# Performance work log

Hardware: AMD Instinct MI355X
Metric: run time of the kernel (lower is better)

## Reference

```python
import jax, jax.numpy as jnp
import numpy as np

N = 1_000_000          # number of fusion candidate pairs
H, W = 200, 70400      # sparse buffer dims hard-coded in the module
FILL = -9999999.0


def _init_conv(k, co, ci):
    # torch Conv2d default init: U(-1/sqrt(fan_in), 1/sqrt(fan_in)), 1x1 kernel
    bound = 1.0 / np.sqrt(ci)
    kw, kb = jax.random.split(k)
    w = jax.random.uniform(kw, (co, ci), jnp.float32, -bound, bound)
    b = jax.random.uniform(kb, (co,), jnp.float32, -bound, bound)
    return w, b


def setup_inputs() -> dict:
    key = jax.random.key(0)
    ks = jax.random.split(key, 7)
    input_1 = jax.random.normal(ks[0], (1, 4, 1, N), dtype=jnp.float32)
    idx0 = jax.random.randint(ks[1], (N,), 0, H)   # row in [0,200)
    idx1 = jax.random.randint(ks[2], (N,), 0, W)   # col in [0,70400)
    tensor_index = jnp.stack([idx0, idx1], axis=1).astype(jnp.int64)
    w1, b1 = _init_conv(ks[3], 18, 4)
    w2, b2 = _init_conv(ks[4], 36, 18)
    w3, b3 = _init_conv(ks[5], 36, 36)
    w4, b4 = _init_conv(ks[6], 1, 36)
    return dict(input_1=input_1, tensor_index=tensor_index,
                w1=w1, b1=b1, w2=w2, b2=b2, w3=w3, b3=b3, w4=w4, b4=b4)


def _fuse_2d_3d(x, w1, b1, w2, b2, w3, b3, w4, b4):
    # x: (4, N); 1x1 convs over a (1,C,1,N) tensor == per-point channel matmuls
    h = jax.nn.relu(w1 @ x + b1[:, None])
    h = jax.nn.relu(w2 @ h + b2[:, None])
    h = jax.nn.relu(w3 @ h + b3[:, None])
    return w4 @ h + b4[:, None]  # (1, N)


def reference(input_1, tensor_index, w1, b1, w2, b2, w3, b3, w4, b4):
    base = jnp.full((1, H, W), FILL, dtype=input_1.dtype)

    def scatter_branch(_):
        feat = _fuse_2d_3d(input_1[0, :, 0, :], w1, b1, w2, b2, w3, b3, w4, b4)  # (1, N)
        out = base.at[:, tensor_index[:, 0], tensor_index[:, 1]].set(feat)
        return out, jnp.int32(1)

    def empty_branch(_):
        return base, jnp.int32(0)

    out_1, flag = jax.lax.cond(tensor_index[0, 0] == -1,
                               empty_branch, scatter_branch, None)
    # MaxPool2d([200,1]) over (C=1,H=200,W) -> max over H; squeeze+reshape -> (1, W, 1)
    x = jnp.max(out_1, axis=1)            # (1, W)
    return x.reshape(1, -1, 1), flag
```

## Files before the change

### kernel.cpp

```cpp
#include <hip/hip_runtime.h>

#define N_PTS 1000000
#define H_DIM 200
#define W_DIM 70400
#define FILL_V -9999999.0f

#define COUNTS_BYTES ((size_t)W_DIM * sizeof(int))
#define WPACK_ELEMS  6656
#define WPACK_BYTES  ((size_t)WPACK_ELEMS * 2)

typedef __attribute__((ext_vector_type(4))) float f32x4;
typedef __attribute__((ext_vector_type(8))) short bf16x8;

__device__ __forceinline__ unsigned bperm_u(unsigned src_lane, unsigned v) {
    return (unsigned)__builtin_amdgcn_ds_bpermute((int)(src_lane << 2), (int)v);
}
__device__ __forceinline__ unsigned cvt_pk_bf16(float lo, float hi) {
    unsigned d;
    asm("v_cvt_pk_bf16_f32 %0, %1, %2" : "=v"(d) : "v"(lo), "v"(hi));
    return d;
}
__device__ __forceinline__ bf16x8 mk_frag(unsigned d0, unsigned d1,
                                          unsigned d2, unsigned d3) {
    union { unsigned u[4]; bf16x8 s; } u;
    u.u[0] = d0; u.u[1] = d1; u.u[2] = d2; u.u[3] = d3;
    return u.s;
}

__global__ void __launch_bounds__(256) pack_weights_kernel(
    const float* __restrict__ w1, const float* __restrict__ b1,
    const float* __restrict__ w2, const float* __restrict__ b2,
    const float* __restrict__ w3, const float* __restrict__ b3,
    const float* __restrict__ w4, const float* __restrict__ b4,
    unsigned short* __restrict__ wp)
{
    for (int idx = threadIdx.x; idx < WPACK_ELEMS; idx += 256) {
        const int rem  = idx & 511;
        const int lane = rem >> 3, j = rem & 7;
        const int c16 = lane & 15, gk = lane >> 4;
        const int kloc = gk * 8 + j;
        float v = 0.0f;
        if (idx < 1024) {
            const int row = (idx >> 9) * 16 + c16, k = kloc;
            if (row < 18) v = (k < 4) ? w1[row * 4 + k] : (k == 4 ? b1[row] : 0.0f);
        } else if (idx < 2560) {
            const int row = ((idx - 1024) >> 9) * 16 + c16;
            const int f = (j < 4) ? (4 * gk + j) : (16 + 4 * gk + (j - 4));
            if (row < 36) v = (f < 18) ? w2[row * 18 + f] : (f == 18 ? b2[row] : 0.0f);
        } else if (idx < 5632) {
            const int f = (idx - 2560) >> 9;
            const int row = (f >> 1) * 16 + c16, k = (f & 1) * 32 + kloc;
            if (row < 36) v = (k < 36) ? w3[row * 36 + k] : (k == 36 ? b3[row] : 0.0f);
        } else {
            const int row = c16, k = ((idx - 5632) >> 9) * 32 + kloc;
            if (row == 0) v = (k < 36) ? w4[k] : (k == 36 ? b4[0] : 0.0f);
        }
        const unsigned b = __float_as_uint(v);
        wp[idx] = (unsigned short)((b + 0x7FFFu + ((b >> 16) & 1u)) >> 16);
    }
}

__global__ void __launch_bounds__(256) mlp_scatter_kernel(
    const float* __restrict__ input,
    const int* __restrict__ tindex,
    const unsigned short* __restrict__ wp,
    int* __restrict__ counts,
    uint2* __restrict__ list,
    int maxk)
{
    if (tindex[0] == -1) return;

    const int l   = threadIdx.x & 63;
    const int wav = (blockIdx.x * 256 + threadIdx.x) >> 6;
    const int base = wav << 6;
    if (base >= N_PTS) return;
    const int i = base + l;
    const int c16 = l & 15, g = l >> 4;

    const int2 hw = ((const int2*)tindex)[i];
    const int pos = atomicAdd(&counts[hw.y], 1);

    const bf16x8* __restrict__ wf = (const bf16x8*)wp;
    const bf16x8 A1_0 = wf[0 * 64 + l], A1_1 = wf[1 * 64 + l];
    const bf16x8 A2_0 = wf[2 * 64 + l], A2_1 = wf[3 * 64 + l], A2_2 = wf[4 * 64 + l];
    const bf16x8 A3_00 = wf[5 * 64 + l], A3_01 = wf[6 * 64 + l];
    const bf16x8 A3_10 = wf[7 * 64 + l], A3_11 = wf[8 * 64 + l];
    const bf16x8 A3_20 = wf[9 * 64 + l], A3_21 = wf[10 * 64 + l];
    const bf16x8 A4_0 = wf[11 * 64 + l], A4_1 = wf[12 * 64 + l];

    const f32x4 zf = {0.0f, 0.0f, 0.0f, 0.0f};

    const float x0 = input[0 * N_PTS + i], x1 = input[1 * N_PTS + i];
    const float x2 = input[2 * N_PTS + i], x3 = input[3 * N_PTS + i];
    const unsigned xp01 = cvt_pk_bf16(x0, x1);
    const unsigned xp23 = cvt_pk_bf16(x2, x3);

    unsigned P1[4][2][2];
#pragma unroll
    for (int t = 0; t < 4; ++t) {
        const unsigned srcl = (unsigned)(16 * t + c16);
        const unsigned bx0 = bperm_u(srcl, xp01);
        const unsigned bx1 = bperm_u(srcl, xp23);
        const unsigned d0 = (g == 0) ? bx0 : 0u;
        const unsigned d1 = (g == 0) ? bx1 : 0u;
        const unsigned d2 = (g == 0) ? 0x3F80u : 0u;
        const bf16x8 B = mk_frag(d0, d1, d2, 0u);
        const f32x4 D0 = __builtin_amdgcn_mfma_f32_16x16x32_bf16(A1_0, B, zf, 0, 0, 0);
        const f32x4 D1 = __builtin_amdgcn_mfma_f32_16x16x32_bf16(A1_1, B, zf, 0, 0, 0);
        P1[t][0][0] = cvt_pk_bf16(fmaxf(D0.x, 0.f), fmaxf(D0.y, 0.f));
        P1[t][0][1] = cvt_pk_bf16(fmaxf(D0.z, 0.f), fmaxf(D0.w, 0.f));
        P1[t][1][0] = cvt_pk_bf16(fmaxf(D1.x, 0.f), fmaxf(D1.y, 0.f));
        P1[t][1][1] = cvt_pk_bf16(fmaxf(D1.z, 0.f), fmaxf(D1.w, 0.f));
    }

    unsigned P2[4][3][2];
#pragma unroll
    for (int t = 0; t < 4; ++t) {
        const unsigned d0 = P1[t][0][0];
        const unsigned d1 = P1[t][0][1];
        const unsigned d2 = P1[t][1][0];
        const unsigned d3 = (g == 0) ? 0x3F80u
                                     : P1[t][1][1];
        const bf16x8 B = mk_frag(d0, d1, d2, d3);
        const f32x4 D0 = __builtin_amdgcn_mfma_f32_16x16x32_bf16(A2_0, B, zf, 0, 0, 0);
        const f32x4 D1 = __builtin_amdgcn_mfma_f32_16x16x32_bf16(A2_1, B, zf, 0, 0, 0);
        const f32x4 D2 = __builtin_amdgcn_mfma_f32_16x16x32_bf16(A2_2, B, zf, 0, 0, 0);
        P2[t][0][0] = cvt_pk_bf16(fmaxf(D0.x, 0.f), fmaxf(D0.y, 0.f));
        P2[t][0][1] = cvt_pk_bf16(fmaxf(D0.z, 0.f), fmaxf(D0.w, 0.f));
        P2[t][1][0] = cvt_pk_bf16(fmaxf(D1.x, 0.f), fmaxf(D1.y, 0.f));
        P2[t][1][1] = cvt_pk_bf16(fmaxf(D1.z, 0.f), fmaxf(D1.w, 0.f));
        P2[t][2][0] = cvt_pk_bf16(fmaxf(D2.x, 0.f), fmaxf(D2.y, 0.f));
        P2[t][2][1] = cvt_pk_bf16(fmaxf(D2.z, 0.f), fmaxf(D2.w, 0.f));
    }

    unsigned P3[4][3][2];
#pragma unroll
    for (int t = 0; t < 4; ++t) {
        unsigned dk0[4], dk1[4];
#pragma unroll
        for (int p = 0; p < 4; ++p) {
            const int Rl = (4 * g + p) & 7;
            const unsigned srcl = (unsigned)(c16 + 16 * (Rl >> 1));
            const unsigned lo = bperm_u(srcl, P2[t][0][p & 1]);
            const unsigned hi = bperm_u(srcl, P2[t][1][p & 1]);
            const unsigned m2 = bperm_u(srcl, P2[t][2][p & 1]);
            dk0[p] = (4 * g + p < 8) ? lo : hi;
            dk1[p] = (4 * g + p < 8) ? m2 : 0u;
        }
        if (g == 0) dk1[2] = (dk1[2] & 0xFFFF0000u) | 0x3F80u;
        const bf16x8 B0 = mk_frag(dk0[0], dk0[1], dk0[2], dk0[3]);
        const bf16x8 B1 = mk_frag(dk1[0], dk1[1], dk1[2], dk1[3]);
        f32x4 D0 = __builtin_amdgcn_mfma_f32_16x16x32_bf16(A3_00, B0, zf, 0, 0, 0);
        D0 = __builtin_amdgcn_mfma_f32_16x16x32_bf16(A3_01, B1, D0, 0, 0, 0);
        f32x4 D1 = __builtin_amdgcn_mfma_f32_16x16x32_bf16(A3_10, B0, zf, 0, 0, 0);
        D1 = __builtin_amdgcn_mfma_f32_16x16x32_bf16(A3_11, B1, D1, 0, 0, 0);
        f32x4 D2 = __builtin_amdgcn_mfma_f32_16x16x32_bf16(A3_20, B0, zf, 0, 0, 0);
        D2 = __builtin_amdgcn_mfma_f32_16x16x32_bf16(A3_21, B1, D2, 0, 0, 0);
        P3[t][0][0] = cvt_pk_bf16(fmaxf(D0.x, 0.f), fmaxf(D0.y, 0.f));
        P3[t][0][1] = cvt_pk_bf16(fmaxf(D0.z, 0.f), fmaxf(D0.w, 0.f));
        P3[t][1][0] = cvt_pk_bf16(fmaxf(D1.x, 0.f), fmaxf(D1.y, 0.f));
        P3[t][1][1] = cvt_pk_bf16(fmaxf(D1.z, 0.f), fmaxf(D1.w, 0.f));
        P3[t][2][0] = cvt_pk_bf16(fmaxf(D2.x, 0.f), fmaxf(D2.y, 0.f));
        P3[t][2][1] = cvt_pk_bf16(fmaxf(D2.z, 0.f), fmaxf(D2.w, 0.f));
    }

    float vout[4];
#pragma unroll
    for (int t = 0; t < 4; ++t) {
        unsigned dk0[4], dk1[4];
#pragma unroll
        for (int p = 0; p < 4; ++p) {
            const int Rl = (4 * g + p) & 7;
            const unsigned srcl = (unsigned)(c16 + 16 * (Rl >> 1));
            const unsigned lo = bperm_u(srcl, P3[t][0][p & 1]);
            const unsigned hi = bperm_u(srcl, P3[t][1][p & 1]);
            const unsigned m2 = bperm_u(srcl, P3[t][2][p & 1]);
            dk0[p] = (4 * g + p < 8) ? lo : hi;
            dk1[p] = (4 * g + p < 8) ? m2 : 0u;
        }
        if (g == 0) dk1[2] = (dk1[2] & 0xFFFF0000u) | 0x3F80u;
        const bf16x8 B0 = mk_frag(dk0[0], dk0[1], dk0[2], dk0[3]);
        const bf16x8 B1 = mk_frag(dk1[0], dk1[1], dk1[2], dk1[3]);
        f32x4 D = __builtin_amdgcn_mfma_f32_16x16x32_bf16(A4_0, B0, zf, 0, 0, 0);
        D = __builtin_amdgcn_mfma_f32_16x16x32_bf16(A4_1, B1, D, 0, 0, 0);
        vout[t] = D.x;
    }

    const unsigned r0 = bperm_u((unsigned)c16, __float_as_uint(vout[0]));
    const unsigned r1 = bperm_u((unsigned)c16, __float_as_uint(vout[1]));
    const unsigned r2 = bperm_u((unsigned)c16, __float_as_uint(vout[2]));
    const unsigned r3 = bperm_u((unsigned)c16, __float_as_uint(vout[3]));
    const unsigned vr = (g < 2) ? ((g == 0) ? r0 : r1) : ((g == 2) ? r2 : r3);

    if (pos < maxk) {
        uint2 e;
        e.x = vr;
        e.y = ((unsigned)i << 8) | (unsigned)hw.x;
        list[(size_t)hw.y * maxk + pos] = e;
    }
}

__device__ __forceinline__ void lds_wave_fence() {
    asm volatile("s_waitcnt lgkmcnt(0)" ::: "memory");
}

__global__ void __launch_bounds__(256) colmax_kernel(
    const int* __restrict__ tindex,
    const int* __restrict__ counts,
    const uint2* __restrict__ list,
    float* __restrict__ out,
    int maxk)
{
    __shared__ unsigned rowwin[4][200];
    const int lane = threadIdx.x;
    const int y    = threadIdx.y;
    unsigned* tbl = rowwin[y];

    const bool empty = (tindex[0] == -1);

    if (blockIdx.x == 0 && lane == 0 && y == 0)
        out[W_DIM] = empty ? 0.0f : 1.0f;

    tbl[lane]       = 0u;
    tbl[lane + 64]  = 0u;
    tbl[lane + 128] = 0u;
    if (lane < 8) tbl[lane + 192] = 0u;
    lds_wave_fence();

    const int step = gridDim.x * 4;
    for (int w = blockIdx.x * 4 + y; w < W_DIM; w += step) {
        int c = 0;
        if (!empty) {
            c = counts[w];
            if (c > maxk) c = maxk;
        }

        uint2 e = make_uint2(0u, 0u);
        const bool have = (lane < c);
        float v = FILL_V;
        if (have) {
            e = list[(size_t)w * maxk + lane];
            atomicMax(&tbl[e.y & 0xFFu], e.y);
        }
        lds_wave_fence();
        if (have) {
            if (tbl[e.y & 0xFFu] == e.y)
                v = __uint_as_float(e.x);
            tbl[e.y & 0xFFu] = 0u;
        }
        lds_wave_fence();

#pragma unroll
        for (int off = 32; off > 0; off >>= 1)
            v = fmaxf(v, __shfl_down(v, off, 64));

        if (lane == 0) out[w] = v;
    }
}

extern "C" void kernel_launch(void* const* d_in, const int* in_sizes, int n_in,
                              void* d_out, int out_size, void* d_ws, size_t ws_size,
                              hipStream_t stream) {
    const float* input  = (const float*)d_in[0];
    const int*   tindex = (const int*)d_in[1];
    const float* w1 = (const float*)d_in[2];
    const float* b1 = (const float*)d_in[3];
    const float* w2 = (const float*)d_in[4];
    const float* b2 = (const float*)d_in[5];
    const float* w3 = (const float*)d_in[6];
    const float* b3 = (const float*)d_in[7];
    const float* w4 = (const float*)d_in[8];
    const float* b4 = (const float*)d_in[9];
    float* out = (float*)d_out;

    int*            counts = (int*)d_ws;
    unsigned short* wpack  = (unsigned short*)((char*)d_ws + COUNTS_BYTES);
    uint2*          list   = (uint2*)((char*)d_ws + COUNTS_BYTES + WPACK_BYTES);

    size_t head = COUNTS_BYTES + WPACK_BYTES;
    size_t avail = (ws_size > head) ? ws_size - head : 0;
    int maxk = (int)(avail / ((size_t)W_DIM * sizeof(uint2)));
    if (maxk > 64) maxk = 64;
    if (maxk < 1)  maxk = 1;

    (void)hipMemsetAsync(counts, 0, COUNTS_BYTES, stream);

    pack_weights_kernel<<<1, 256, 0, stream>>>(w1, b1, w2, b2, w3, b3, w4, b4, wpack);

    mlp_scatter_kernel<<<(N_PTS / 64 + 3) / 4, 256, 0, stream>>>(
        input, tindex, wpack, counts, list, maxk);

    colmax_kernel<<<2200, dim3(64, 4), 0, stream>>>(
        tindex, counts, list, out, maxk);
}
```

Measured before the change: 166.5 us.

## Split scatter list into 4-byte keys plus a dense feature array

The MLP kernel now writes each point's output value to a dense per-point feat array with coalesced stores, and scatters only a 4-byte packed (index,row) key into the per-column bucket list instead of an 8-byte pair. The column-max kernel reads the key, then gathers the feature value from feat by point index. This halves the scattered write and read traffic on the bucket list. In exchange it adds a dense 4MB write and a random gather read in the reduction kernel. The smaller entries can also let maxk be larger for a given workspace size.

```diff
diff --git a/kernel.cpp b/kernel.cpp
--- a/kernel.cpp
+++ b/kernel.cpp
@@ -8,6 +8,7 @@
 #define COUNTS_BYTES ((size_t)W_DIM * sizeof(int))
 #define WPACK_ELEMS  6656
 #define WPACK_BYTES  ((size_t)WPACK_ELEMS * 2)
+#define FEAT_BYTES   ((size_t)N_PTS * 4)
 
 typedef __attribute__((ext_vector_type(4))) float f32x4;
 typedef __attribute__((ext_vector_type(8))) short bf16x8;
@@ -65,7 +66,8 @@
     const int* __restrict__ tindex,
     const unsigned short* __restrict__ wp,
     int* __restrict__ counts,
-    uint2* __restrict__ list,
+    unsigned* __restrict__ feat,
+    unsigned* __restrict__ list4,
     int maxk)
 {
     if (tindex[0] == -1) return;
@@ -101,10 +103,9 @@
         const unsigned srcl = (unsigned)(16 * t + c16);
         const unsigned bx0 = bperm_u(srcl, xp01);
         const unsigned bx1 = bperm_u(srcl, xp23);
-        const unsigned d0 = (g == 0) ? bx0 : 0u;
-        const unsigned d1 = (g == 0) ? bx1 : 0u;
-        const unsigned d2 = (g == 0) ? 0x3F80u : 0u;
-        const bf16x8 B = mk_frag(d0, d1, d2, 0u);
+        const bf16x8 B = mk_frag((g == 0) ? bx0 : 0u,
+                                 (g == 0) ? bx1 : 0u,
+                                 (g == 0) ? 0x3F80u : 0u, 0u);
         const f32x4 D0 = __builtin_amdgcn_mfma_f32_16x16x32_bf16(A1_0, B, zf, 0, 0, 0);
         const f32x4 D1 = __builtin_amdgcn_mfma_f32_16x16x32_bf16(A1_1, B, zf, 0, 0, 0);
         P1[t][0][0] = cvt_pk_bf16(fmaxf(D0.x, 0.f), fmaxf(D0.y, 0.f));
@@ -116,12 +117,8 @@
     unsigned P2[4][3][2];
 #pragma unroll
     for (int t = 0; t < 4; ++t) {
-        const unsigned d0 = P1[t][0][0];
-        const unsigned d1 = P1[t][0][1];
-        const unsigned d2 = P1[t][1][0];
-        const unsigned d3 = (g == 0) ? 0x3F80u
-                                     : P1[t][1][1];
-        const bf16x8 B = mk_frag(d0, d1, d2, d3);
+        const bf16x8 B = mk_frag(P1[t][0][0], P1[t][0][1], P1[t][1][0],
+                                 (g == 0) ? 0x3F80u : P1[t][1][1]);
         const f32x4 D0 = __builtin_amdgcn_mfma_f32_16x16x32_bf16(A2_0, B, zf, 0, 0, 0);
         const f32x4 D1 = __builtin_amdgcn_mfma_f32_16x16x32_bf16(A2_1, B, zf, 0, 0, 0);
         const f32x4 D2 = __builtin_amdgcn_mfma_f32_16x16x32_bf16(A2_2, B, zf, 0, 0, 0);
@@ -192,12 +189,9 @@
     const unsigned r3 = bperm_u((unsigned)c16, __float_as_uint(vout[3]));
     const unsigned vr = (g < 2) ? ((g == 0) ? r0 : r1) : ((g == 2) ? r2 : r3);
 
-    if (pos < maxk) {
-        uint2 e;
-        e.x = vr;
-        e.y = ((unsigned)i << 8) | (unsigned)hw.x;
-        list[(size_t)hw.y * maxk + pos] = e;
-    }
+    feat[i] = vr;
+    if (pos < maxk)
+        list4[(size_t)hw.y * maxk + pos] = ((unsigned)i << 8) | (unsigned)hw.x;
 }
 
 __device__ __forceinline__ void lds_wave_fence() {
@@ -207,7 +201,8 @@
 __global__ void __launch_bounds__(256) colmax_kernel(
     const int* __restrict__ tindex,
     const int* __restrict__ counts,
-    const uint2* __restrict__ list,
+    const unsigned* __restrict__ list4,
+    const unsigned* __restrict__ feat,
     float* __restrict__ out,
     int maxk)
 {
@@ -235,18 +230,19 @@
             if (c > maxk) c = maxk;
         }
 
-        uint2 e = make_uint2(0u, 0u);
+        unsigned e4 = 0u, fb = 0u;
         const bool have = (lane < c);
         float v = FILL_V;
         if (have) {
-            e = list[(size_t)w * maxk + lane];
-            atomicMax(&tbl[e.y & 0xFFu], e.y);
+            e4 = list4[(size_t)w * maxk + lane];
+            fb = feat[e4 >> 8];
+            atomicMax(&tbl[e4 & 0xFFu], e4);
         }
         lds_wave_fence();
         if (have) {
-            if (tbl[e.y & 0xFFu] == e.y)
-                v = __uint_as_float(e.x);
-            tbl[e.y & 0xFFu] = 0u;
+            if (tbl[e4 & 0xFFu] == e4)
+                v = __uint_as_float(fb);
+            tbl[e4 & 0xFFu] = 0u;
         }
         lds_wave_fence();
 
@@ -275,11 +271,12 @@
 
     int*            counts = (int*)d_ws;
     unsigned short* wpack  = (unsigned short*)((char*)d_ws + COUNTS_BYTES);
-    uint2*          list   = (uint2*)((char*)d_ws + COUNTS_BYTES + WPACK_BYTES);
-
-    size_t head = COUNTS_BYTES + WPACK_BYTES;
+    unsigned*       feat   = (unsigned*)((char*)d_ws + COUNTS_BYTES + WPACK_BYTES);
+    unsigned*       list4  = (unsigned*)((char*)d_ws + COUNTS_BYTES + WPACK_BYTES + FEAT_BYTES);
+
+    size_t head = COUNTS_BYTES + WPACK_BYTES + FEAT_BYTES;
     size_t avail = (ws_size > head) ? ws_size - head : 0;
-    int maxk = (int)(avail / ((size_t)W_DIM * sizeof(uint2)));
+    int maxk = (int)(avail / ((size_t)W_DIM * sizeof(unsigned)));
     if (maxk > 64) maxk = 64;
     if (maxk < 1)  maxk = 1;
 
@@ -288,8 +285,8 @@
     pack_weights_kernel<<<1, 256, 0, stream>>>(w1, b1, w2, b2, w3, b3, w4, b4, wpack);
 
     mlp_scatter_kernel<<<(N_PTS / 64 + 3) / 4, 256, 0, stream>>>(
-        input, tindex, wpack, counts, list, maxk);
+        input, tindex, wpack, counts, feat, list4, maxk);
 
     colmax_kernel<<<2200, dim3(64, 4), 0, stream>>>(
-        tindex, counts, list, out, maxk);
-}
+        tindex, counts, list4, feat, out, maxk);
+}
```

Result: no change. 167.6 us (+0.7%).
